# Kernel tuning notes

Hardware: AMD Instinct MI355X
Metric: run time of the kernel (lower is better)

## Reference

```python
import jax, jax.numpy as jnp
import numpy as np

HIDDEN = 1024
HEADS = 16
HEAD = HIDDEN // HEADS
B, S = 2, 2048


def setup_inputs() -> dict:
    key = jax.random.key(0)
    ks = jax.random.split(key, 8)
    query = jax.random.normal(ks[0], (B, S, HIDDEN), dtype=jnp.float32)
    key_t = jax.random.normal(ks[1], (B, S, HIDDEN), dtype=jnp.float32)
    value = jax.random.normal(ks[2], (B, S, HIDDEN), dtype=jnp.float32)
    # causal mask, broadcastable over batch and heads; 0 -> masked (-inf)
    mask = jnp.tril(jnp.ones((S, S), dtype=jnp.int32))[None, None, :, :]
    # torch Linear weights are [out_features, in_features]
    scale = 0.02
    Wq = jax.random.normal(ks[3], (HIDDEN, HIDDEN), dtype=jnp.float32) * scale
    Wk = jax.random.normal(ks[4], (HIDDEN, HIDDEN), dtype=jnp.float32) * scale
    Wv = jax.random.normal(ks[5], (HIDDEN, HIDDEN), dtype=jnp.float32) * scale
    Wo = jax.random.normal(ks[6], (HIDDEN, HIDDEN), dtype=jnp.float32) * scale
    bo = jax.random.normal(ks[7], (HIDDEN,), dtype=jnp.float32) * scale
    return {"query": query, "key": key_t, "value": value, "mask": mask,
            "Wq": Wq, "Wk": Wk, "Wv": Wv, "Wo": Wo, "bo": bo}


def reference(query, key, value, mask, Wq, Wk, Wv, Wo, bo):
    b = query.shape[0]
    # Linear (no bias): x @ W^T, then split into heads -> [b, h, s, d]
    def heads(x, W):
        y = jnp.einsum('bse,oe->bso', x, W)
        return y.reshape(b, -1, HEADS, HEAD).transpose(0, 2, 1, 3)
    Q = heads(query, Wq)
    K = heads(key, Wk)
    V = heads(value, Wv)
    inv_scale = 1.0 / jnp.sqrt(jnp.float32(HEAD))
    scores = jnp.einsum('bhqd,bhkd->bhqk', Q, K) * inv_scale  # [b,h,s,s]
    scores = jnp.where(mask == 0, -jnp.inf, scores)
    attn = jax.nn.softmax(scores, axis=-1)
    x = jnp.einsum('bhqk,bhkd->bhqd', attn, V)
    x = x.transpose(0, 2, 1, 3).reshape(b, -1, HIDDEN)
    return jnp.einsum('bse,oe->bso', x, Wo) + bo
```

## Files before the change

kernel.cpp:

```cpp
#include <hip/hip_runtime.h>


typedef __attribute__((ext_vector_type(8))) short short8;
typedef __attribute__((ext_vector_type(4))) float f32x4;
typedef unsigned int u32;
typedef unsigned short u16;

__device__ inline f32x4 mfma16(short8 a, short8 b, f32x4 c) {
    return __builtin_amdgcn_mfma_f32_16x16x32_bf16(a, b, c, 0, 0, 0);
}
__device__ inline u16 f2bf(float f) {
    union { float f; u32 u; } v; v.f = f;
    u32 r = v.u + 0x7fff + ((v.u >> 16) & 1);
    return (u16)(r >> 16);
}
__device__ inline void gll16(void* lds, const void* g) {
    __builtin_amdgcn_global_load_lds((const __attribute__((address_space(1))) u32*)g,
                                     (__attribute__((address_space(3))) u32*)lds,
                                     16, 0, 0);
}
__device__ inline u32 pkbf(float hi, float lo) {
    return __builtin_amdgcn_perm(__float_as_uint(hi), __float_as_uint(lo),
                                 0x07060302u);
}

__global__ __launch_bounds__(256)
void cvt_all(const float* __restrict__ q, const float* __restrict__ k,
             const float* __restrict__ v, const float* __restrict__ wq,
             const float* __restrict__ wk, const float* __restrict__ wv,
             const float* __restrict__ wo,
             u16* __restrict__ q16, u16* __restrict__ k16,
             u16* __restrict__ v16, u16* __restrict__ w16) {
    const size_t QKV = 1u << 22;
    const size_t WSZ = 1u << 20;
    size_t base = ((size_t)blockIdx.x * 256 + threadIdx.x) * 8;
    const float* src; u16* dst; size_t off; float scale = 1.0f;
    if (base < QKV)            { src = q; dst = q16; off = base;
                                 scale = 0.125f * 1.44269504f; }
    else if (base < 2 * QKV)   { src = k; dst = k16; off = base - QKV;     }
    else if (base < 3 * QKV)   { src = v; dst = v16; off = base - 2 * QKV; }
    else {
        size_t wb = base - 3 * QKV;
        int wi = (int)(wb >> 20); off = wb & (WSZ - 1);
        src = wi == 0 ? wq : wi == 1 ? wk : wi == 2 ? wv : wo;
        dst = w16 + (size_t)wi * WSZ;
    }
    float4 f0 = *(const float4*)(src + off);
    float4 f1 = *(const float4*)(src + off + 4);
    short8 s = { (short)f2bf(f0.x * scale), (short)f2bf(f0.y * scale),
                 (short)f2bf(f0.z * scale), (short)f2bf(f0.w * scale),
                 (short)f2bf(f1.x * scale), (short)f2bf(f1.y * scale),
                 (short)f2bf(f1.z * scale), (short)f2bf(f1.w * scale) };
    *(short8*)(dst + off) = s;
}

__global__ __launch_bounds__(256)
void gemm_qkv(const u16* __restrict__ q16, const u16* __restrict__ k16,
              const u16* __restrict__ v16, const u16* __restrict__ w16,
              u16* __restrict__ Qg, u16* __restrict__ Kg, u16* __restrict__ Vt) {
    const int K = 1024;
    __shared__ u16 As[3][128 * 32];
    __shared__ u16 Bs[3][128 * 32];
    const int z = blockIdx.z;
    const u16* A = z == 0 ? q16 : z == 1 ? k16 : v16;
    const u16* W = w16 + (size_t)z * (1u << 20);

    const int tid = threadIdx.x, lane = tid & 63, w = tid >> 6;
    const int ln15 = lane & 15, quad = lane >> 4;
    const int fr = (ln15 >> 1) & 3;
    const int lrow = lane >> 2;
    const int lcs = (((lane & 3) ^ ((lane >> 3) & 3)) << 3);
    const int m0 = blockIdx.y * 128, n0 = blockIdx.x * 128;
    const int wm = (w >> 1) * 64, wn = (w & 1) * 64;

    f32x4 acc[4][4] = {};

    #pragma unroll
    for (int t = 0; t < 2; ++t)
        #pragma unroll
        for (int c = 0; c < 2; ++c) {
            gll16(&As[t][(w * 32 + c * 16) * 32],
                  &A[(size_t)(m0 + w * 32 + c * 16 + lrow) * K + t * 32 + lcs]);
            gll16(&Bs[t][(w * 32 + c * 16) * 32],
                  &W[(size_t)(n0 + w * 32 + c * 16 + lrow) * K + t * 32 + lcs]);
        }

    int cur = 0;
    for (int t = 0; t < 32; ++t) {
        if (t < 31) {
            __asm__ volatile("s_waitcnt vmcnt(4)" ::: "memory");
        } else {
            __asm__ volatile("s_waitcnt vmcnt(0)" ::: "memory");
        }
        __builtin_amdgcn_s_barrier();
        __builtin_amdgcn_sched_barrier(0);

        if (t < 30) {
            const int k0 = (t + 2) * 32;
            const int nb = (cur + 2 >= 3) ? cur - 1 : cur + 2;
            #pragma unroll
            for (int c = 0; c < 2; ++c) {
                gll16(&As[nb][(w * 32 + c * 16) * 32],
                      &A[(size_t)(m0 + w * 32 + c * 16 + lrow) * K + k0 + lcs]);
                gll16(&Bs[nb][(w * 32 + c * 16) * 32],
                      &W[(size_t)(n0 + w * 32 + c * 16 + lrow) * K + k0 + lcs]);
            }
        }
        __builtin_amdgcn_sched_barrier(0);

        short8 a[4], b[4];
        #pragma unroll
        for (int mt = 0; mt < 4; ++mt)
            a[mt] = *(const short8*)&As[cur][(wm + mt * 16 + ln15) * 32 +
                                            ((quad ^ fr) << 3)];
        #pragma unroll
        for (int nt = 0; nt < 4; ++nt)
            b[nt] = *(const short8*)&Bs[cur][(wn + nt * 16 + ln15) * 32 +
                                            ((quad ^ fr) << 3)];
        #pragma unroll
        for (int mt = 0; mt < 4; ++mt)
            #pragma unroll
            for (int nt = 0; nt < 4; ++nt)
                acc[mt][nt] = mfma16(a[mt], b[nt], acc[mt][nt]);

        cur = (cur == 2) ? 0 : cur + 1;
    }

    #pragma unroll
    for (int mt = 0; mt < 4; ++mt)
        #pragma unroll
        for (int nt = 0; nt < 4; ++nt)
            #pragma unroll
            for (int r = 0; r < 4; ++r) {
                int m = m0 + wm + mt * 16 + quad * 4 + r;
                int n = n0 + wn + nt * 16 + ln15;
                u16 hv = f2bf(acc[mt][nt][r]);
                if (z == 2) {
                    int b_ = m >> 11, s_ = m & 2047, h_ = n >> 6, d_ = n & 63;
                    int kl = s_ & 63;
                    int sp = (s_ & ~63) + (kl & 15) * 4 + (kl >> 4);
                    Vt[((size_t)(b_ * 16 + h_) * 64 + d_) * 2048 + sp] = hv;
                } else {
                    u16* dst = z ? Kg : Qg;
                    dst[(size_t)m * 1024 + n] = hv;
                }
            }
}

__global__ __launch_bounds__(256)
void gemm_out(const u16* __restrict__ A, const u16* __restrict__ W,
              const float* __restrict__ bias, float* __restrict__ out) {
    const int K = 1024;
    __shared__ u16 As[2][64 * 64];
    __shared__ u16 Bs[2][64 * 64];
    const int id = blockIdx.x;
    const int by = id >> 4, bx = id & 15;

    const int tid = threadIdx.x, lane = tid & 63, w = tid >> 6;
    const int ln15 = lane & 15, quad = lane >> 4, s7 = ln15 & 7;
    const int lr = lane >> 3;
    const int lcs = (((lane & 7) ^ lr) << 3);
    const int m0 = by * 64, n0 = bx * 64;
    const int wm = (w & 1) * 32, wn = (w >> 1) * 32;

    f32x4 acc[2][2] = {};

    #pragma unroll
    for (int c = 0; c < 2; ++c) {
        gll16(&As[0][(w * 16 + c * 8) * 64],
              &A[(size_t)(m0 + w * 16 + c * 8 + lr) * K + lcs]);
        gll16(&Bs[0][(w * 16 + c * 8) * 64],
              &W[(size_t)(n0 + w * 16 + c * 8 + lr) * K + lcs]);
    }

    for (int i = 0; i < 16; ++i) {
        const int cur = i & 1, nb = cur ^ 1;
        __asm__ volatile("s_waitcnt vmcnt(0)" ::: "memory");
        __builtin_amdgcn_s_barrier();
        __builtin_amdgcn_sched_barrier(0);

        if (i < 15) {
            const int k0 = (i + 1) * 64;
            #pragma unroll
            for (int c = 0; c < 2; ++c) {
                gll16(&As[nb][(w * 16 + c * 8) * 64],
                      &A[(size_t)(m0 + w * 16 + c * 8 + lr) * K + k0 + lcs]);
                gll16(&Bs[nb][(w * 16 + c * 8) * 64],
                      &W[(size_t)(n0 + w * 16 + c * 8 + lr) * K + k0 + lcs]);
            }
        }
        __builtin_amdgcn_sched_barrier(0);

        #pragma unroll
        for (int kh = 0; kh < 2; ++kh) {
            short8 a[2], b[2];
            #pragma unroll
            for (int mt = 0; mt < 2; ++mt)
                a[mt] = *(const short8*)&As[cur][(wm + mt * 16 + ln15) * 64 +
                                                (((kh * 4 + quad) ^ s7) << 3)];
            #pragma unroll
            for (int nt = 0; nt < 2; ++nt)
                b[nt] = *(const short8*)&Bs[cur][(wn + nt * 16 + ln15) * 64 +
                                                (((kh * 4 + quad) ^ s7) << 3)];
            #pragma unroll
            for (int mt = 0; mt < 2; ++mt)
                #pragma unroll
                for (int nt = 0; nt < 2; ++nt)
                    acc[mt][nt] = mfma16(a[mt], b[nt], acc[mt][nt]);
        }
    }

    #pragma unroll
    for (int mt = 0; mt < 2; ++mt)
        #pragma unroll
        for (int nt = 0; nt < 2; ++nt)
            #pragma unroll
            for (int r = 0; r < 4; ++r) {
                int m = m0 + wm + mt * 16 + quad * 4 + r;
                int n = n0 + wn + nt * 16 + ln15;
                out[(size_t)m * 1024 + n] = acc[mt][nt][r] + bias[n];
            }
}

__global__ __launch_bounds__(256)
void attn3(const u16* __restrict__ Qg, const u16* __restrict__ Kg,
           const u16* __restrict__ Vt, u16* __restrict__ Xb) {
    __shared__ u16 Kl[2][64 * 64];
    __shared__ u16 Vl[2][64 * 64];
    __shared__ u16 Pl[4][16 * 64];

    const int id = blockIdx.x;
    const int bh = id & 31;
    const int kk = id >> 5, jj = kk >> 3, mm = kk & 7;
    const int qt = (jj == 0) ? 31 - mm : (jj == 1) ? mm
                 : (jj == 2) ? 23 - mm : 8 + mm;
    const int b = bh >> 4, h = bh & 15;
    const int tid = threadIdx.x, lane = tid & 63, w = tid >> 6;
    const int ln15 = lane & 15, quad = lane >> 4, s7 = ln15 & 7;
    const int lr = lane >> 3;
    const int lcs = (((lane & 7) ^ lr) << 3);
    const u16* Kbase = Kg + (size_t)b * 2048 * 1024 + h * 64;
    const u16* Vbase = Vt + (size_t)bh * 64 * 2048;
    const float M0L = 8.65617025f;
    const int q0 = qt * 64;

    const u16* qrow = Qg + (size_t)(b * 2048 + q0 + w * 16 + ln15) * 1024 + h * 64;
    short8 aq0 = *(const short8*)(qrow + quad * 8);
    short8 aq1 = *(const short8*)(qrow + 32 + quad * 8);
    __asm__ volatile("s_waitcnt vmcnt(0)" ::: "memory");

    f32x4 o[4] = {};
    float lsum[4] = {0.f, 0.f, 0.f, 0.f};

    #pragma unroll
    for (int c = 0; c < 2; ++c) {
        const int r0 = w * 16 + c * 8;
        gll16(&Kl[0][r0 * 64], Kbase + (size_t)(r0 + lr) * 1024 + lcs);
        gll16(&Vl[0][r0 * 64], Vbase + (size_t)(r0 + lr) * 2048 + lcs);
    }

    for (int kt = 0; kt <= qt; ++kt) {
        const int cur = kt & 1, nb = cur ^ 1;
        __asm__ volatile("s_waitcnt vmcnt(0)" ::: "memory");
        __builtin_amdgcn_s_barrier();
        __builtin_amdgcn_sched_barrier(0);

        if (kt < qt) {
            const int nk = (kt + 1) * 64;
            #pragma unroll
            for (int c = 0; c < 2; ++c) {
                const int r0 = w * 16 + c * 8;
                gll16(&Kl[nb][r0 * 64], Kbase + (size_t)(nk + r0 + lr) * 1024 + lcs);
                gll16(&Vl[nb][r0 * 64], Vbase + (size_t)(r0 + lr) * 2048 + nk + lcs);
            }
        }
        __builtin_amdgcn_sched_barrier(0);

        f32x4 sc[4];
        __builtin_amdgcn_s_setprio(1);
        #pragma unroll
        for (int ct = 0; ct < 4; ++ct) {
            short8 b0 = *(const short8*)&Kl[cur][(ct * 16 + ln15) * 64 +
                                                ((quad ^ s7) << 3)];
            short8 b1 = *(const short8*)&Kl[cur][(ct * 16 + ln15) * 64 +
                                                (((4 + quad) ^ s7) << 3)];
            f32x4 c = {};
            c = mfma16(aq0, b0, c);
            c = mfma16(aq1, b1, c);
            sc[ct] = c;
        }
        __builtin_amdgcn_s_setprio(0);

        const bool diag = (kt == qt);
        #pragma unroll
        for (int r = 0; r < 4; ++r) {
            float s0 = sc[0][r], s1 = sc[1][r], s2 = sc[2][r], s3 = sc[3][r];
            if (diag) {
                const int qq = w * 16 + quad * 4 + r;
                s0 = (ln15      <= qq) ? s0 : -1e30f;
                s1 = (16 + ln15 <= qq) ? s1 : -1e30f;
                s2 = (32 + ln15 <= qq) ? s2 : -1e30f;
                s3 = (48 + ln15 <= qq) ? s3 : -1e30f;
            }
            float p0 = __builtin_amdgcn_exp2f(s0 - M0L);
            float p1 = __builtin_amdgcn_exp2f(s1 - M0L);
            float p2 = __builtin_amdgcn_exp2f(s2 - M0L);
            float p3 = __builtin_amdgcn_exp2f(s3 - M0L);
            uint2 pw = make_uint2(pkbf(p1, p0), pkbf(p3, p2));
            *(uint2*)&Pl[w][(quad * 4 + r) * 64 + ln15 * 4] = pw;
            lsum[r] += (p0 + p1) + (p2 + p3);
        }

        __asm__ volatile("s_waitcnt lgkmcnt(0)" ::: "memory");
        short8 ap0 = *(const short8*)&Pl[w][ln15 * 64 + quad * 8];
        short8 ap1 = *(const short8*)&Pl[w][ln15 * 64 + 32 + quad * 8];

        __builtin_amdgcn_s_setprio(1);
        #pragma unroll
        for (int dt = 0; dt < 4; ++dt) {
            short8 bv0 = *(const short8*)&Vl[cur][(dt * 16 + ln15) * 64 +
                                                 ((quad ^ s7) << 3)];
            short8 bv1 = *(const short8*)&Vl[cur][(dt * 16 + ln15) * 64 +
                                                 (((4 + quad) ^ s7) << 3)];
            o[dt] = mfma16(ap0, bv0, o[dt]);
            o[dt] = mfma16(ap1, bv1, o[dt]);
        }
        __builtin_amdgcn_s_setprio(0);
    }

    #pragma unroll
    for (int r = 0; r < 4; ++r) {
        float l = lsum[r];
        #pragma unroll
        for (int off = 1; off < 16; off <<= 1)
            l += __shfl_xor(l, off);
        lsum[r] = l;
    }
    #pragma unroll
    for (int dt = 0; dt < 4; ++dt)
        #pragma unroll
        for (int r = 0; r < 4; ++r) {
            int q = q0 + w * 16 + quad * 4 + r;
            Xb[(size_t)(b * 2048 + q) * 1024 + h * 64 + dt * 16 + ln15] =
                f2bf(o[dt][r] / lsum[r]);
        }
}

extern "C" void kernel_launch(void* const* d_in, const int* in_sizes, int n_in,
                              void* d_out, int out_size, void* d_ws, size_t ws_size,
                              hipStream_t stream) {
    const float* query = (const float*)d_in[0];
    const float* key   = (const float*)d_in[1];
    const float* value = (const float*)d_in[2];
    const float* Wq = (const float*)d_in[4];
    const float* Wk = (const float*)d_in[5];
    const float* Wv = (const float*)d_in[6];
    const float* Wo = (const float*)d_in[7];
    const float* bo = (const float*)d_in[8];
    float* out = (float*)d_out;

    u16* ws  = (u16*)d_ws;
    const size_t T = 1ull << 22;
    u16* q16 = ws;
    u16* k16 = ws + T;
    u16* v16 = ws + 2 * T;
    u16* w16 = ws + 3 * T;
    u16* Qg  = ws + 4 * T;
    u16* Kg  = ws + 5 * T;
    u16* Vt  = (u16*)d_out;
    u16* Xb  = q16;
    const size_t WSZ = 1ull << 20;

    cvt_all<<<8192, 256, 0, stream>>>(query, key, value, Wq, Wk, Wv, Wo,
                                      q16, k16, v16, w16);

    gemm_qkv<<<dim3(8, 32, 3), 256, 0, stream>>>(q16, k16, v16, w16, Qg, Kg, Vt);

    attn3<<<1024, 256, 0, stream>>>(Qg, Kg, Vt, Xb);

    gemm_out<<<1024, 256, 0, stream>>>(Xb, w16 + 3 * WSZ, bo, out);
}
```

Measured before the change: 219.9 us.

## Pre-tile bf16 activations and QKV weights into contiguous 128x32 blocks

The conversion kernel now writes Q/K/V activations and the Wq/Wk/Wv weights in a blocked layout, where each 128-row by 32-column tile is stored contiguously. The QKV GEMM's async global-to-LDS loads then read contiguous 8KB chunks instead of 64-byte pieces strided across rows. This targets DRAM/TLB locality and coalescing in the GEMM load path. The cost is scattered 16-byte writes in the conversion kernel, and Wo keeps its row-major layout.

After: 218.6 us. No clear change (-0.6%).

```diff
diff --git a/kernel.cpp b/kernel.cpp
--- a/kernel.cpp
+++ b/kernel.cpp
@@ -35,6 +35,7 @@
     const size_t WSZ = 1u << 20;
     size_t base = ((size_t)blockIdx.x * 256 + threadIdx.x) * 8;
     const float* src; u16* dst; size_t off; float scale = 1.0f;
+    bool tiled = true;
     if (base < QKV)            { src = q; dst = q16; off = base;
                                  scale = 0.125f * 1.44269504f; }
     else if (base < 2 * QKV)   { src = k; dst = k16; off = base - QKV;     }
@@ -44,6 +45,7 @@
         int wi = (int)(wb >> 20); off = wb & (WSZ - 1);
         src = wi == 0 ? wq : wi == 1 ? wk : wi == 2 ? wv : wo;
         dst = w16 + (size_t)wi * WSZ;
+        tiled = (wi != 3);
     }
     float4 f0 = *(const float4*)(src + off);
     float4 f1 = *(const float4*)(src + off + 4);
@@ -51,14 +53,19 @@
                  (short)f2bf(f0.z * scale), (short)f2bf(f0.w * scale),
                  (short)f2bf(f1.x * scale), (short)f2bf(f1.y * scale),
                  (short)f2bf(f1.z * scale), (short)f2bf(f1.w * scale) };
-    *(short8*)(dst + off) = s;
+    size_t didx = off;
+    if (tiled) {
+        size_t m = off >> 10, kk = off & 1023;
+        didx = ((m >> 7) * 131072) + ((kk >> 5) * 4096)
+             + ((m & 127) * 32) + (kk & 31);
+    }
+    *(short8*)(dst + didx) = s;
 }
 
 __global__ __launch_bounds__(256)
 void gemm_qkv(const u16* __restrict__ q16, const u16* __restrict__ k16,
               const u16* __restrict__ v16, const u16* __restrict__ w16,
               u16* __restrict__ Qg, u16* __restrict__ Kg, u16* __restrict__ Vt) {
-    const int K = 1024;
     __shared__ u16 As[3][128 * 32];
     __shared__ u16 Bs[3][128 * 32];
     const int z = blockIdx.z;
@@ -71,6 +78,8 @@
     const int lrow = lane >> 2;
     const int lcs = (((lane & 3) ^ ((lane >> 3) & 3)) << 3);
     const int m0 = blockIdx.y * 128, n0 = blockIdx.x * 128;
+    const size_t mbase = (size_t)blockIdx.y * 131072;
+    const size_t nbase = (size_t)blockIdx.x * 131072;
     const int wm = (w >> 1) * 64, wn = (w & 1) * 64;
 
     f32x4 acc[4][4] = {};
@@ -79,10 +88,11 @@
     for (int t = 0; t < 2; ++t)
         #pragma unroll
         for (int c = 0; c < 2; ++c) {
-            gll16(&As[t][(w * 32 + c * 16) * 32],
-                  &A[(size_t)(m0 + w * 32 + c * 16 + lrow) * K + t * 32 + lcs]);
-            gll16(&Bs[t][(w * 32 + c * 16) * 32],
-                  &W[(size_t)(n0 + w * 32 + c * 16 + lrow) * K + t * 32 + lcs]);
+            const int r0 = w * 32 + c * 16;
+            gll16(&As[t][r0 * 32],
+                  &A[mbase + (size_t)t * 4096 + (r0 + lrow) * 32 + lcs]);
+            gll16(&Bs[t][r0 * 32],
+                  &W[nbase + (size_t)t * 4096 + (r0 + lrow) * 32 + lcs]);
         }
 
     int cur = 0;
@@ -96,14 +106,15 @@
         __builtin_amdgcn_sched_barrier(0);
 
         if (t < 30) {
-            const int k0 = (t + 2) * 32;
+            const size_t kb = (size_t)(t + 2) * 4096;
             const int nb = (cur + 2 >= 3) ? cur - 1 : cur + 2;
             #pragma unroll
             for (int c = 0; c < 2; ++c) {
-                gll16(&As[nb][(w * 32 + c * 16) * 32],
-                      &A[(size_t)(m0 + w * 32 + c * 16 + lrow) * K + k0 + lcs]);
-                gll16(&Bs[nb][(w * 32 + c * 16) * 32],
-                      &W[(size_t)(n0 + w * 32 + c * 16 + lrow) * K + k0 + lcs]);
+                const int r0 = w * 32 + c * 16;
+                gll16(&As[nb][r0 * 32],
+                      &A[mbase + kb + (r0 + lrow) * 32 + lcs]);
+                gll16(&Bs[nb][r0 * 32],
+                      &W[nbase + kb + (r0 + lrow) * 32 + lcs]);
             }
         }
         __builtin_amdgcn_sched_barrier(0);
```
